# Optimization experiments

Hardware: AMD Instinct MI355X
Metric: run time of the kernel (lower is better)

## Reference

```python
import jax, jax.numpy as jnp
import numpy as np

I_DECAY = 0.95
STAG_THRESH = 0.95
MAX_GATE = 0.6
MIN_I_GATE = 0.25
EPS = 1e-12


def setup_inputs() -> dict:
    key = jax.random.key(0)
    ks = jax.random.split(key, 9)
    B, T, D_IN, D_OUT = 4, 2048, 2048, 2048
    x = jax.random.normal(ks[0], (B, T, D_IN), dtype=jnp.float32)
    s = 1.0 / np.sqrt(D_IN)
    Wp = jax.random.uniform(ks[1], (D_IN, D_OUT), jnp.float32, -s, s)
    Wi = jax.random.uniform(ks[2], (D_IN, D_OUT), jnp.float32, -s, s) * 0.3
    Wd = jax.random.uniform(ks[3], (D_IN, D_OUT), jnp.float32, -s, s) * 0.3
    gate_w = jax.random.uniform(ks[4], (D_IN, 3), jnp.float32, -s, s)
    gate_b = jnp.array([0.5, 0.0, 0.0], dtype=jnp.float32)
    kick_vec = jax.random.normal(ks[5], (D_OUT,), dtype=jnp.float32) * 0.01
    kick_w = jax.random.uniform(ks[6], (D_IN, 1), jnp.float32, -s, s)
    kick_b = jnp.full((1,), -2.0, dtype=jnp.float32)
    bias = jnp.zeros((D_OUT,), dtype=jnp.float32)
    return {"x": x, "Wp": Wp, "Wi": Wi, "Wd": Wd, "gate_w": gate_w,
            "gate_b": gate_b, "kick_vec": kick_vec, "kick_w": kick_w,
            "kick_b": kick_b, "bias": bias}


def _ema_integral(x, decay):
    # x: [B,T,D] -> time-major scan; integral[0] = x[0]
    xt = jnp.swapaxes(x, 0, 1)  # [T,B,D]

    def step(carry, xcur):
        new = decay * carry + (1.0 - decay) * xcur
        return new, new

    init = xt[0]
    _, rest = jax.lax.scan(step, init, xt[1:])
    integral = jnp.concatenate([init[None], rest], axis=0)
    return jnp.swapaxes(integral, 0, 1)  # [B,T,D]


def reference(x, Wp, Wi, Wd, gate_w, gate_b, kick_vec, kick_w, kick_b, bias):
    B, T, D = x.shape
    # --- EMA integral (linear recurrence over T) ---
    integral = _ema_integral(x, I_DECAY)

    # --- stagnation-aware derivative ---
    diff = jnp.concatenate(
        [jnp.zeros_like(x[:, :1]), x[:, 1:] - x[:, :-1]], axis=1)
    x_norm = x / jnp.maximum(
        jnp.linalg.norm(x, axis=-1, keepdims=True), EPS)
    cos_sim = jnp.concatenate(
        [jnp.zeros((B, 1), x.dtype),
         jnp.sum(x_norm[:, 1:] * x_norm[:, :-1], axis=-1)], axis=1)  # [B,T]
    stagnation = (cos_sim > STAG_THRESH).astype(x.dtype)
    kick_strength = jax.nn.sigmoid(
        jnp.einsum('btd,do->bto', x, kick_w) + kick_b)[..., 0]  # [B,T]
    derivative = diff + (stagnation * kick_strength)[..., None] * kick_vec

    # --- gates: softmax -> clamp max -> clamp I min -> renormalize ---
    g = jax.nn.softmax(jnp.einsum('btd,dg->btg', x, gate_w) + gate_b, axis=-1)
    g = jnp.minimum(g, MAX_GATE)
    g = g.at[..., 1].set(jnp.maximum(g[..., 1], MIN_I_GATE))
    g = g / jnp.sum(g, axis=-1, keepdims=True)

    out = (g[..., 0:1] * jnp.einsum('btd,do->bto', x, Wp)
           + g[..., 1:2] * jnp.einsum('btd,do->bto', integral, Wi)
           + g[..., 2:3] * jnp.einsum('btd,do->bto', derivative, Wd))
    return out + bias
```

## Files before the change

### kernel.cpp

```cpp
#include <hip/hip_runtime.h>

#define DH 2048
#define TT 2048
#define BB 4
#define MROWS 8192
#define NZ 6144
#define NCH 128
#define LCH 16
#define LAM 0.44012667f
#define LAM2 1.982646e-06f

typedef __attribute__((ext_vector_type(8))) short bf16x8;
typedef __attribute__((ext_vector_type(4))) float f32x4;

__device__ __forceinline__ unsigned short f2bf(float f) {
  union { float f; unsigned int u; } v; v.f = f;
  unsigned int u = v.u;
  return (unsigned short)((u + 0x7FFFu + ((u >> 16) & 1u)) >> 16);
}
__device__ __forceinline__ float bf2f(unsigned short u) {
  union { unsigned int i; float f; } v; v.i = ((unsigned int)u) << 16;
  return v.f;
}
__device__ __forceinline__ void gld16(const unsigned short* g, unsigned short* l) {
  __builtin_amdgcn_global_load_lds((const __attribute__((address_space(1))) void*)g,
                                   (__attribute__((address_space(3))) void*)l, 16, 0, 0);
}

__global__ __launch_bounds__(256) void prep_w(const float* __restrict__ Wp,
                                              const float* __restrict__ Wi,
                                              const float* __restrict__ Wd,
                                              const float* __restrict__ kick_vec,
                                              unsigned short* __restrict__ Wt,
                                              float* __restrict__ kvWd) {
  __shared__ float tile[64][65];
  int bid = blockIdx.x;
  int mat = bid >> 10;
  int t2 = bid & 1023;
  int dt = (t2 >> 5) * 64;
  int ot = (t2 & 31) * 64;
  const float* W = (mat == 0) ? Wp : ((mat == 1) ? Wi : Wd);
  int nbase = mat * DH;
  int tid = threadIdx.x;
  int r = tid >> 4;
  int c4 = (tid & 15) * 4;
#pragma unroll
  for (int i = 0; i < 4; ++i) {
    int rr = r + i * 16;
    float4 v = *(const float4*)&W[(size_t)(dt + rr) * DH + ot + c4];
    tile[rr][c4 + 0] = v.x; tile[rr][c4 + 1] = v.y;
    tile[rr][c4 + 2] = v.z; tile[rr][c4 + 3] = v.w;
  }
  __syncthreads();
  int o = tid >> 3;
  int d8 = (tid & 7) * 8;
#pragma unroll
  for (int pass = 0; pass < 2; ++pass) {
    int oo = o + pass * 32;
    union { unsigned short u[8]; uint4 v; } pk;
#pragma unroll
    for (int i = 0; i < 8; ++i) pk.u[i] = f2bf(tile[d8 + i][oo]);
    *(uint4*)&Wt[(size_t)(nbase + ot + oo) * DH + dt + d8] = pk.v;
  }
  if (mat == 2 && tid < 64) {
    float s = 0.f;
#pragma unroll 8
    for (int dd = 0; dd < 64; ++dd) s += kick_vec[dt + dd] * tile[dd][tid];
    atomicAdd(&kvWd[ot + tid], s);
  }
}

__global__ __launch_bounds__(256) void conv_x(const float* __restrict__ x,
                                              const float* __restrict__ gate_w,
                                              const float* __restrict__ gate_b,
                                              const float* __restrict__ kick_w,
                                              const float* __restrict__ kick_b,
                                              float* __restrict__ rs,
                                              unsigned short* __restrict__ A) {
  int r = blockIdx.x;
  int t = r & (TT - 1);
  const float* xr = x + (size_t)r * DH;
  const float* xq = xr - DH;
  const bool hp = (t != 0);
  int tid = threadIdx.x;
  float a0 = 0, a1 = 0, a2 = 0, ak = 0, axx = 0, apx = 0, app = 0;
#pragma unroll
  for (int it = 0; it < 2; ++it) {
    int d0 = (tid + it * 256) * 4;
    float4 xv = *(const float4*)(xr + d0);
    float4 pv = hp ? *(const float4*)(xq + d0) : make_float4(0.f, 0.f, 0.f, 0.f);
    float4 q0 = *(const float4*)(gate_w + (size_t)d0 * 3);
    float4 q1 = *(const float4*)(gate_w + (size_t)d0 * 3 + 4);
    float4 q2 = *(const float4*)(gate_w + (size_t)d0 * 3 + 8);
    float4 kw = *(const float4*)(kick_w + d0);
    float xa[4] = {xv.x, xv.y, xv.z, xv.w};
    float pa[4] = {pv.x, pv.y, pv.z, pv.w};
    a0 += xa[0] * q0.x + xa[1] * q0.w + xa[2] * q1.z + xa[3] * q2.y;
    a1 += xa[0] * q0.y + xa[1] * q1.x + xa[2] * q1.w + xa[3] * q2.z;
    a2 += xa[0] * q0.z + xa[1] * q1.y + xa[2] * q2.x + xa[3] * q2.w;
    ak += xa[0] * kw.x + xa[1] * kw.y + xa[2] * kw.z + xa[3] * kw.w;
    union { unsigned short u[4]; uint2 v; } pk;
#pragma unroll
    for (int j = 0; j < 4; ++j) {
      axx += xa[j] * xa[j];
      apx += xa[j] * pa[j];
      app += pa[j] * pa[j];
      pk.u[j] = f2bf(xa[j]);
    }
    *(uint2*)&A[(size_t)r * DH + d0] = pk.v;
  }
#pragma unroll
  for (int off = 32; off > 0; off >>= 1) {
    a0 += __shfl_xor(a0, off); a1 += __shfl_xor(a1, off);
    a2 += __shfl_xor(a2, off); ak += __shfl_xor(ak, off);
    axx += __shfl_xor(axx, off); apx += __shfl_xor(apx, off);
    app += __shfl_xor(app, off);
  }
  __shared__ float red[4][7];
  int wv = tid >> 6;
  if ((tid & 63) == 0) {
    red[wv][0] = a0; red[wv][1] = a1; red[wv][2] = a2; red[wv][3] = ak;
    red[wv][4] = axx; red[wv][5] = apx; red[wv][6] = app;
  }
  __syncthreads();
  if (tid == 0) {
    float v[7];
#pragma unroll
    for (int i = 0; i < 7; ++i) v[i] = red[0][i] + red[1][i] + red[2][i] + red[3][i];
    float l0 = v[0] + gate_b[0], l1 = v[1] + gate_b[1], l2 = v[2] + gate_b[2];
    float mx = fmaxf(l0, fmaxf(l1, l2));
    float e0 = expf(l0 - mx), e1 = expf(l1 - mx), e2 = expf(l2 - mx);
    float inv = 1.f / (e0 + e1 + e2);
    float G0 = fminf(e0 * inv, 0.6f);
    float G1 = fminf(e1 * inv, 0.6f);
    float G2 = fminf(e2 * inv, 0.6f);
    G1 = fmaxf(G1, 0.25f);
    float inv2 = 1.f / (G0 + G1 + G2);
    G0 *= inv2; G1 *= inv2; G2 *= inv2;
    float ks = 1.f / (1.f + expf(-(v[3] + kick_b[0])));
    float nn = fmaxf(sqrtf(v[4]), 1e-12f) * fmaxf(sqrtf(v[6]), 1e-12f);
    float cs = hp ? (v[5] / nn) : 0.f;
    float cc = (cs > 0.95f) ? (G2 * ks) : 0.f;
    *(float4*)(rs + (size_t)r * 4) = make_float4(G0, G1, G2, cc);
  }
}


#define BAR __builtin_amdgcn_s_barrier()
#define VMW6 asm volatile("s_waitcnt vmcnt(6)" ::: "memory")
#define VMW4 asm volatile("s_waitcnt vmcnt(4)" ::: "memory")
#define VMW0 asm volatile("s_waitcnt vmcnt(0)" ::: "memory")
#define LGK8 asm volatile("s_waitcnt lgkmcnt(8)" ::: "memory")
#define LGK0 asm volatile("s_waitcnt lgkmcnt(0)" ::: "memory")

#define ST_A(bf, h, kt) do { \
  gld16(pA + (size_t)((h) * 64) * DH + (kt) * 64,       lA + (bf) * 16384 + (h) * 8192 + ldsW); \
  gld16(pA + (size_t)((h) * 64 + 128) * DH + (kt) * 64, lA + (bf) * 16384 + (h) * 8192 + 4096 + ldsW); \
} while (0)
#define ST_B(bf, g, kt) do { \
  gld16(pB + (size_t)((g) * 32) * DH + (kt) * 64,       lB + (bf) * 16384 + (g) * 8192 + ldsW); \
  gld16(pB + (size_t)((g) * 32 + 128) * DH + (kt) * 64, lB + (bf) * 16384 + (g) * 8192 + 4096 + ldsW); \
} while (0)

#define RD_A(bf, h) do { \
  const unsigned short* p_ = lA + (bf) * 16384 + (h) * 8192 + aRd; \
  _Pragma("unroll") \
  for (int mi_ = 0; mi_ < 4; ++mi_) { \
    av[mi_][0] = *(const bf16x8*)(p_ + mi_ * 1024 + kph0); \
    av[mi_][1] = *(const bf16x8*)(p_ + mi_ * 1024 + kph1); \
  } \
} while (0)
#define RD_B(bf, g) do { \
  const unsigned short* p_ = lB + (bf) * 16384 + (g) * 8192 + bRd; \
  _Pragma("unroll") \
  for (int ni_ = 0; ni_ < 2; ++ni_) { \
    bv[g][ni_][0] = *(const bf16x8*)(p_ + ni_ * 1024 + kph0); \
    bv[g][ni_][1] = *(const bf16x8*)(p_ + ni_ * 1024 + kph1); \
  } \
} while (0)

#define MM(h, g) do { \
  __builtin_amdgcn_s_setprio(1); \
  _Pragma("unroll") \
  for (int mi_ = 0; mi_ < 4; ++mi_) { \
    _Pragma("unroll") \
    for (int ni_ = 0; ni_ < 2; ++ni_) { \
      f32x4 c_ = acc[(h) * 4 + mi_][(g) * 2 + ni_]; \
      c_ = __builtin_amdgcn_mfma_f32_16x16x32_bf16(av[mi_][0], bv[g][ni_][0], c_, 0, 0, 0); \
      c_ = __builtin_amdgcn_mfma_f32_16x16x32_bf16(av[mi_][1], bv[g][ni_][1], c_, 0, 0, 0); \
      acc[(h) * 4 + mi_][(g) * 2 + ni_] = c_; \
    } \
  } \
  __builtin_amdgcn_s_setprio(0); \
} while (0)

__global__ __launch_bounds__(512, 2) void gemm_kernel(const unsigned short* __restrict__ A,
                                                      const unsigned short* __restrict__ Bt,
                                                      unsigned short* __restrict__ Z,
                                                      unsigned short* __restrict__ cpb) {
  __shared__ __align__(16) unsigned short lA[2 * 16384];
  __shared__ __align__(16) unsigned short lB[2 * 16384];
  const int tid = threadIdx.x;
  const int wave = tid >> 6, lane = tid & 63;
  const int bid = blockIdx.x;
  const int xcd = bid & 7;
  const int loc = bid >> 3;
  const int mblk = xcd * 4 + (loc & 3);
  const int nblk = loc >> 2;
  const int m0 = mblk * 256, n0 = nblk * 256;

  const int wm = wave >> 2, wn = wave & 3;
  const int rA = lane & 15, q = lane >> 4, sw = lane & 7;
  const int kph0 = ((0 + q) ^ sw) * 8;
  const int kph1 = ((4 + q) ^ sw) * 8;
  const int aRd = wm * 4096 + rA * 64;
  const int bRd = wn * 2048 + rA * 64;

  const int trow = tid >> 3;
  const int tcol = ((tid & 7) ^ (trow & 7)) * 8;
  const unsigned short* pA = A + (size_t)(m0 + trow) * DH + tcol;
  const unsigned short* pB = Bt + (size_t)(n0 + (trow >> 5) * 64 + (trow & 31)) * DH + tcol;
  const int ldsW = wave * 512;

  bf16x8 av[4][2];
  bf16x8 bv[2][2][2];
  f32x4 acc[8][4] = {};

  ST_A(0, 0, 0); ST_B(0, 0, 0); ST_B(0, 1, 0); ST_A(0, 1, 0);
  ST_A(1, 0, 1); ST_B(1, 0, 1); ST_B(1, 1, 1);
  VMW6; BAR;

#pragma unroll 1
  for (int i = 0; i < 15; ++i) {
    const int t1 = 2 * i + 1, t2 = 2 * i + 2, t3 = 2 * i + 3;
    RD_A(0, 0); RD_B(0, 0); LGK8; BAR; LGK0; MM(0, 0); ST_A(1, 1, t1);
    RD_B(0, 1);                   BAR; LGK0; MM(0, 1); ST_A(0, 0, t2);
    RD_A(0, 1);                   BAR; LGK0; MM(1, 0); ST_B(0, 0, t2);
                            VMW4; BAR;       MM(1, 1); ST_B(0, 1, t2);
    RD_A(1, 0); RD_B(1, 0); LGK8; BAR; LGK0; MM(0, 0); ST_A(0, 1, t2);
    RD_B(1, 1);                   BAR; LGK0; MM(0, 1); ST_A(1, 0, t3);
    RD_A(1, 1);                   BAR; LGK0; MM(1, 0); ST_B(1, 0, t3);
                            VMW4; BAR;       MM(1, 1); ST_B(1, 1, t3);
  }
  RD_A(0, 0); RD_B(0, 0); LGK8; BAR; LGK0; MM(0, 0); ST_A(1, 1, 31);
  RD_B(0, 1);                   BAR; LGK0; MM(0, 1);
  RD_A(0, 1);                   BAR; LGK0; MM(1, 0);
                          VMW0; BAR;       MM(1, 1);
  RD_A(1, 0); RD_B(1, 0); LGK8; BAR; LGK0; MM(0, 0);
  RD_B(1, 1);                   BAR; LGK0; MM(0, 1);
  RD_A(1, 1);                   BAR; LGK0; MM(1, 0);
                                           MM(1, 1);

  const int mbase = m0 + wm * 128;
  const int nbase = n0 + wn * 64;

  if (nblk >= 8 && nblk < 16) {
    float w12 = (q == 3) ? 1.0f : (q == 2) ? 0.81450625f
              : (q == 1) ? 0.66342043f : 0.54036009f;
    w12 *= 0.05f;
#pragma unroll
    for (int mi = 0; mi < 8; ++mi) {
      const int mrow = mbase + mi * 16;
      const int bb = mrow >> 11;
      const int chh = (mrow >> 4) & (NCH - 1);
      const bool first = (chh == 0);
#pragma unroll
      for (int ni = 0; ni < 4; ++ni) {
        float v0 = acc[mi][ni][0];
        float s = ((v0 * 0.95f + acc[mi][ni][1]) * 0.95f + acc[mi][ni][2]) * 0.95f
                  + acc[mi][ni][3];
        if (first && q == 0) s += 19.0f * 0.857375f * v0;
        s *= w12;
        s += __shfl_xor(s, 16);
        s += __shfl_xor(s, 32);
        if (q == 0) {
          int nloc = nbase + ni * 16 + rA - 2048;
          cpb[((size_t)bb * NCH + chh) * DH + nloc] = f2bf(s);
        }
      }
    }
  }

#pragma unroll
  for (int mi = 0; mi < 8; ++mi) {
#pragma unroll
    for (int rg = 0; rg < 4; ++rg) {
      const int m = mbase + mi * 16 + q * 4 + rg;
#pragma unroll
      for (int ni = 0; ni < 4; ++ni) {
        const int n = nbase + ni * 16 + rA;
        Z[(size_t)m * NZ + n] = f2bf(acc[mi][ni][rg]);
      }
    }
  }
}

#undef BAR
#undef VMW6
#undef VMW4
#undef VMW0
#undef LGK8
#undef LGK0
#undef ST_A
#undef ST_B
#undef RD_A
#undef RD_B
#undef MM

__global__ __launch_bounds__(256) void zi_p1(unsigned short* __restrict__ cpb,
                                             float* __restrict__ gc) {
  int gid = blockIdx.x * 256 + threadIdx.x;
  int n = gid & (DH - 1);
  int g = (gid >> 11) & 7;
  int b = gid >> 14;
  float run = 0.f;
#pragma unroll
  for (int j = 0; j < 16; ++j) {
    size_t idx = ((size_t)b * NCH + g * 16 + j) * DH + n;
    float c = bf2f(cpb[idx]);
    cpb[idx] = f2bf(run);
    run = c + LAM * run;
  }
  gc[((size_t)b * 8 + g) * DH + n] = run;
}

__global__ __launch_bounds__(256) void zi_p2(float* __restrict__ gc) {
  int gid = blockIdx.x * 256 + threadIdx.x;
  int n = gid & (DH - 1);
  int b = gid >> 11;
  float run = 0.f;
#pragma unroll
  for (int g = 0; g < 8; ++g) {
    size_t idx = ((size_t)b * 8 + g) * DH + n;
    float old = gc[idx];
    gc[idx] = run;
    run = old + LAM2 * run;
  }
}

__global__ __launch_bounds__(256) void final_combine(const unsigned short* __restrict__ Z,
                                                     const float* __restrict__ rs,
                                                     const unsigned short* __restrict__ cpb,
                                                     const float* __restrict__ gc,
                                                     const float* __restrict__ kvWd,
                                                     const float* __restrict__ bias,
                                                     float* __restrict__ out) {
  int tid = threadIdx.x;
  int n = blockIdx.y * 1024 + tid * 4;
  int ch = blockIdx.x & (NCH - 1);
  int b = blockIdx.x >> 7;
  int r0 = b * TT + ch * LCH;
  const unsigned short* zb = Z + (size_t)r0 * NZ + n;
  const bool first_chunk = (ch == 0);

  int g = ch >> 4, j = ch & 15;
  float pw = 1.f;
  for (int i = 0; i < j; ++i) pw *= LAM;
  float Pv[4];
  {
    union { unsigned short u[4]; uint2 v; } c;
    c.v = *(const uint2*)&cpb[((size_t)b * NCH + ch) * DH + n];
    float4 gp = *(const float4*)&gc[((size_t)b * 8 + g) * DH + n];
    float gpa[4] = {gp.x, gp.y, gp.z, gp.w};
#pragma unroll
    for (int i = 0; i < 4; ++i) Pv[i] = bf2f(c.u[i]) + pw * gpa[i];
  }
  float kv[4], bz[4];
  {
    float4 k0 = *(const float4*)&kvWd[n];
    float4 b0 = *(const float4*)&bias[n];
    kv[0]=k0.x; kv[1]=k0.y; kv[2]=k0.z; kv[3]=k0.w;
    bz[0]=b0.x; bz[1]=b0.y; bz[2]=b0.z; bz[3]=b0.w;
  }
  float zdp[4];
  if (!first_chunk) {
    union { unsigned short u[4]; uint2 v; } c;
    c.v = *(const uint2*)(zb - NZ + 2 * DH);
#pragma unroll
    for (int i = 0; i < 4; ++i) zdp[i] = bf2f(c.u[i]);
  } else {
#pragma unroll
    for (int i = 0; i < 4; ++i) zdp[i] = 0.f;
  }
  float J[4];
#pragma unroll
  for (int i = 0; i < 4; ++i) J[i] = 0.f;
  float f = 1.f;
  uint2 cp = *(const uint2*)(zb);
  uint2 ci = *(const uint2*)(zb + DH);
  uint2 cd = *(const uint2*)(zb + 2 * DH);
#pragma unroll
  for (int tau = 0; tau < LCH; ++tau) {
    uint2 np, ni, nd;
    if (tau < LCH - 1) {
      const unsigned short* zn = zb + (size_t)(tau + 1) * NZ;
      np = *(const uint2*)(zn);
      ni = *(const uint2*)(zn + DH);
      nd = *(const uint2*)(zn + 2 * DH);
    }
    float4 gg = *(const float4*)&rs[(size_t)(r0 + tau) * 4];
    union { unsigned short u[4]; uint2 v; } up, ui, ud;
    up.v = cp; ui.v = ci; ud.v = cd;
    const bool vfirst = first_chunk && (tau == 0);
    f *= 0.95f;
    float o[4];
#pragma unroll
    for (int i = 0; i < 4; ++i) {
      float xp = bf2f(up.u[i]), xi = bf2f(ui.u[i]), xd = bf2f(ud.u[i]);
      if (vfirst) J[i] = xi;
      else J[i] = 0.95f * J[i] + 0.05f * xi;
      float I = J[i] + f * Pv[i];
      float diff = vfirst ? 0.f : (xd - zdp[i]);
      o[i] = gg.x * xp + gg.y * I + gg.z * diff + gg.w * kv[i] + bz[i];
      zdp[i] = xd;
    }
    *(float4*)(out + (size_t)(r0 + tau) * DH + n) = make_float4(o[0], o[1], o[2], o[3]);
    cp = np; ci = ni; cd = nd;
  }
}

extern "C" void kernel_launch(void* const* d_in, const int* in_sizes, int n_in,
                              void* d_out, int out_size, void* d_ws, size_t ws_size,
                              hipStream_t stream) {
  const float* x        = (const float*)d_in[0];
  const float* Wp       = (const float*)d_in[1];
  const float* Wi       = (const float*)d_in[2];
  const float* Wd       = (const float*)d_in[3];
  const float* gate_w   = (const float*)d_in[4];
  const float* gate_b   = (const float*)d_in[5];
  const float* kick_vec = (const float*)d_in[6];
  const float* kick_w   = (const float*)d_in[7];
  const float* kick_b   = (const float*)d_in[8];
  const float* bias     = (const float*)d_in[9];
  float* out = (float*)d_out;

  char* ws = (char*)d_ws;
  unsigned short* Wt  = (unsigned short*)(ws + 0);
  unsigned short* Z   = (unsigned short*)(ws + 25165824);
  float* rs   = (float*)(ws + 125829120);
  float* kvWd = (float*)(ws + 125960192);
  unsigned short* cpb = (unsigned short*)(ws + 125968384);
  float* gc   = (float*)(ws + 128065536);
  unsigned short* A = (unsigned short*)d_out;
  (void)ws_size; (void)in_sizes; (void)n_in; (void)out_size;

  hipMemsetAsync(kvWd, 0, DH * sizeof(float), stream);
  prep_w<<<dim3(3072), dim3(256), 0, stream>>>(Wp, Wi, Wd, kick_vec, Wt, kvWd);
  conv_x<<<dim3(8192), dim3(256), 0, stream>>>(x, gate_w, gate_b, kick_w, kick_b, rs, A);
  gemm_kernel<<<dim3(768), dim3(512), 0, stream>>>(A, Wt, Z, cpb);
  zi_p1<<<dim3(256), dim3(256), 0, stream>>>(cpb, gc);
  zi_p2<<<dim3(32), dim3(256), 0, stream>>>(gc);
  final_combine<<<dim3(512, 2), dim3(256), 0, stream>>>(Z, rs, cpb, gc, kvWd, bias, out);
}
```

Baseline: 373.3 us.

## Merge prep kernels, drop zi_p2 pass, reorder GEMM LDS stores before waits

Merges the weight-transpose and x-conversion kernels into one launch with a block-index split, which removes one kernel launch and lets the two independent prep jobs overlap. It drops the second-level carry scan kernel and computes the group carry inline in final_combine from the two previous group carries. Because LAM2 is about 2e-6, terms beyond two groups back are treated as negligible, so this is an approximation of the full scan. It also reorders the GEMM main loop so the next global-to-LDS stores are issued right after the barrier and before the LDS wait and MFMA, and removes the partial lgkmcnt(8) wait.

```diff
diff --git a/kernel.cpp b/kernel.cpp
--- a/kernel.cpp
+++ b/kernel.cpp
@@ -27,62 +27,63 @@
                                    (__attribute__((address_space(3))) void*)l, 16, 0, 0);
 }
 
-__global__ __launch_bounds__(256) void prep_w(const float* __restrict__ Wp,
-                                              const float* __restrict__ Wi,
-                                              const float* __restrict__ Wd,
-                                              const float* __restrict__ kick_vec,
-                                              unsigned short* __restrict__ Wt,
-                                              float* __restrict__ kvWd) {
+__global__ __launch_bounds__(256) void prep_conv(const float* __restrict__ Wp,
+                                                 const float* __restrict__ Wi,
+                                                 const float* __restrict__ Wd,
+                                                 const float* __restrict__ kick_vec,
+                                                 unsigned short* __restrict__ Wt,
+                                                 float* __restrict__ kvWd,
+                                                 const float* __restrict__ x,
+                                                 const float* __restrict__ gate_w,
+                                                 const float* __restrict__ gate_b,
+                                                 const float* __restrict__ kick_w,
+                                                 const float* __restrict__ kick_b,
+                                                 float* __restrict__ rs,
+                                                 unsigned short* __restrict__ A) {
   __shared__ float tile[64][65];
+  __shared__ float red[4][7];
   int bid = blockIdx.x;
-  int mat = bid >> 10;
-  int t2 = bid & 1023;
-  int dt = (t2 >> 5) * 64;
-  int ot = (t2 & 31) * 64;
-  const float* W = (mat == 0) ? Wp : ((mat == 1) ? Wi : Wd);
-  int nbase = mat * DH;
   int tid = threadIdx.x;
-  int r = tid >> 4;
-  int c4 = (tid & 15) * 4;
-#pragma unroll
-  for (int i = 0; i < 4; ++i) {
-    int rr = r + i * 16;
-    float4 v = *(const float4*)&W[(size_t)(dt + rr) * DH + ot + c4];
-    tile[rr][c4 + 0] = v.x; tile[rr][c4 + 1] = v.y;
-    tile[rr][c4 + 2] = v.z; tile[rr][c4 + 3] = v.w;
-  }
-  __syncthreads();
-  int o = tid >> 3;
-  int d8 = (tid & 7) * 8;
-#pragma unroll
-  for (int pass = 0; pass < 2; ++pass) {
-    int oo = o + pass * 32;
-    union { unsigned short u[8]; uint4 v; } pk;
-#pragma unroll
-    for (int i = 0; i < 8; ++i) pk.u[i] = f2bf(tile[d8 + i][oo]);
-    *(uint4*)&Wt[(size_t)(nbase + ot + oo) * DH + dt + d8] = pk.v;
-  }
-  if (mat == 2 && tid < 64) {
-    float s = 0.f;
+  if (bid < 3072) {
+    int mat = bid >> 10;
+    int t2 = bid & 1023;
+    int dt = (t2 >> 5) * 64;
+    int ot = (t2 & 31) * 64;
+    const float* W = (mat == 0) ? Wp : ((mat == 1) ? Wi : Wd);
+    int nbase = mat * DH;
+    int r = tid >> 4;
+    int c4 = (tid & 15) * 4;
+#pragma unroll
+    for (int i = 0; i < 4; ++i) {
+      int rr = r + i * 16;
+      float4 v = *(const float4*)&W[(size_t)(dt + rr) * DH + ot + c4];
+      tile[rr][c4 + 0] = v.x; tile[rr][c4 + 1] = v.y;
+      tile[rr][c4 + 2] = v.z; tile[rr][c4 + 3] = v.w;
+    }
+    __syncthreads();
+    int o = tid >> 3;
+    int d8 = (tid & 7) * 8;
+#pragma unroll
+    for (int pass = 0; pass < 2; ++pass) {
+      int oo = o + pass * 32;
+      union { unsigned short u[8]; uint4 v; } pk;
+#pragma unroll
+      for (int i = 0; i < 8; ++i) pk.u[i] = f2bf(tile[d8 + i][oo]);
+      *(uint4*)&Wt[(size_t)(nbase + ot + oo) * DH + dt + d8] = pk.v;
+    }
+    if (mat == 2 && tid < 64) {
+      float s = 0.f;
 #pragma unroll 8
-    for (int dd = 0; dd < 64; ++dd) s += kick_vec[dt + dd] * tile[dd][tid];
-    atomicAdd(&kvWd[ot + tid], s);
-  }
-}
-
-__global__ __launch_bounds__(256) void conv_x(const float* __restrict__ x,
-                                              const float* __restrict__ gate_w,
-                                              const float* __restrict__ gate_b,
-                                              const float* __restrict__ kick_w,
-                                              const float* __restrict__ kick_b,
-                                              float* __restrict__ rs,
-                                              unsigned short* __restrict__ A) {
-  int r = blockIdx.x;
+      for (int dd = 0; dd < 64; ++dd) s += kick_vec[dt + dd] * tile[dd][tid];
+      atomicAdd(&kvWd[ot + tid], s);
+    }
+    return;
+  }
+  int r = bid - 3072;
   int t = r & (TT - 1);
   const float* xr = x + (size_t)r * DH;
   const float* xq = xr - DH;
   const bool hp = (t != 0);
-  int tid = threadIdx.x;
   float a0 = 0, a1 = 0, a2 = 0, ak = 0, axx = 0, apx = 0, app = 0;
 #pragma unroll
   for (int it = 0; it < 2; ++it) {
@@ -116,7 +117,6 @@
     axx += __shfl_xor(axx, off); apx += __shfl_xor(apx, off);
     app += __shfl_xor(app, off);
   }
-  __shared__ float red[4][7];
   int wv = tid >> 6;
   if ((tid & 63) == 0) {
     red[wv][0] = a0; red[wv][1] = a1; red[wv][2] = a2; red[wv][3] = ak;
@@ -150,7 +150,6 @@
 #define VMW6 asm volatile("s_waitcnt vmcnt(6)" ::: "memory")
 #define VMW4 asm volatile("s_waitcnt vmcnt(4)" ::: "memory")
 #define VMW0 asm volatile("s_waitcnt vmcnt(0)" ::: "memory")
-#define LGK8 asm volatile("s_waitcnt lgkmcnt(8)" ::: "memory")
 #define LGK0 asm volatile("s_waitcnt lgkmcnt(0)" ::: "memory")
 
 #define ST_A(bf, h, kt) do { \
@@ -233,23 +232,23 @@
 #pragma unroll 1
   for (int i = 0; i < 15; ++i) {
     const int t1 = 2 * i + 1, t2 = 2 * i + 2, t3 = 2 * i + 3;
-    RD_A(0, 0); RD_B(0, 0); LGK8; BAR; LGK0; MM(0, 0); ST_A(1, 1, t1);
-    RD_B(0, 1);                   BAR; LGK0; MM(0, 1); ST_A(0, 0, t2);
-    RD_A(0, 1);                   BAR; LGK0; MM(1, 0); ST_B(0, 0, t2);
-                            VMW4; BAR;       MM(1, 1); ST_B(0, 1, t2);
-    RD_A(1, 0); RD_B(1, 0); LGK8; BAR; LGK0; MM(0, 0); ST_A(0, 1, t2);
-    RD_B(1, 1);                   BAR; LGK0; MM(0, 1); ST_A(1, 0, t3);
-    RD_A(1, 1);                   BAR; LGK0; MM(1, 0); ST_B(1, 0, t3);
-                            VMW4; BAR;       MM(1, 1); ST_B(1, 1, t3);
-  }
-  RD_A(0, 0); RD_B(0, 0); LGK8; BAR; LGK0; MM(0, 0); ST_A(1, 1, 31);
-  RD_B(0, 1);                   BAR; LGK0; MM(0, 1);
-  RD_A(0, 1);                   BAR; LGK0; MM(1, 0);
-                          VMW0; BAR;       MM(1, 1);
-  RD_A(1, 0); RD_B(1, 0); LGK8; BAR; LGK0; MM(0, 0);
-  RD_B(1, 1);                   BAR; LGK0; MM(0, 1);
-  RD_A(1, 1);                   BAR; LGK0; MM(1, 0);
-                                           MM(1, 1);
+    RD_A(0, 0); RD_B(0, 0); BAR; ST_A(1, 1, t1); LGK0; MM(0, 0);
+    RD_B(0, 1);             BAR; ST_A(0, 0, t2); LGK0; MM(0, 1);
+    RD_A(0, 1);             BAR; ST_B(0, 0, t2); LGK0; MM(1, 0);
+                      VMW4; BAR; ST_B(0, 1, t2);       MM(1, 1);
+    RD_A(1, 0); RD_B(1, 0); BAR; ST_A(0, 1, t2); LGK0; MM(0, 0);
+    RD_B(1, 1);             BAR; ST_A(1, 0, t3); LGK0; MM(0, 1);
+    RD_A(1, 1);             BAR; ST_B(1, 0, t3); LGK0; MM(1, 0);
+                      VMW4; BAR; ST_B(1, 1, t3);       MM(1, 1);
+  }
+  RD_A(0, 0); RD_B(0, 0); BAR; ST_A(1, 1, 31); LGK0; MM(0, 0);
+  RD_B(0, 1);             BAR;                 LGK0; MM(0, 1);
+  RD_A(0, 1);             BAR;                 LGK0; MM(1, 0);
+                    VMW0; BAR;                       MM(1, 1);
+  RD_A(1, 0); RD_B(1, 0); BAR;                 LGK0; MM(0, 0);
+  RD_B(1, 1);             BAR;                 LGK0; MM(0, 1);
+  RD_A(1, 1);             BAR;                 LGK0; MM(1, 0);
+                                                     MM(1, 1);
 
   const int mbase = m0 + wm * 128;
   const int nbase = n0 + wn * 64;
@@ -299,7 +298,6 @@
 #undef VMW6
 #undef VMW4
 #undef VMW0
-#undef LGK8
 #undef LGK0
 #undef ST_A
 #undef ST_B
@@ -322,20 +320,6 @@
     run = c + LAM * run;
   }
   gc[((size_t)b * 8 + g) * DH + n] = run;
-}
-
-__global__ __launch_bounds__(256) void zi_p2(float* __restrict__ gc) {
-  int gid = blockIdx.x * 256 + threadIdx.x;
-  int n = gid & (DH - 1);
-  int b = gid >> 11;
-  float run = 0.f;
-#pragma unroll
-  for (int g = 0; g < 8; ++g) {
-    size_t idx = ((size_t)b * 8 + g) * DH + n;
-    float old = gc[idx];
-    gc[idx] = run;
-    run = old + LAM2 * run;
-  }
 }
 
 __global__ __launch_bounds__(256) void final_combine(const unsigned short* __restrict__ Z,
@@ -360,8 +344,16 @@
   {
     union { unsigned short u[4]; uint2 v; } c;
     c.v = *(const uint2*)&cpb[((size_t)b * NCH + ch) * DH + n];
-    float4 gp = *(const float4*)&gc[((size_t)b * 8 + g) * DH + n];
-    float gpa[4] = {gp.x, gp.y, gp.z, gp.w};
+    float gpa[4] = {0.f, 0.f, 0.f, 0.f};
+    if (g >= 1) {
+      float4 g1 = *(const float4*)&gc[((size_t)b * 8 + g - 1) * DH + n];
+      gpa[0] = g1.x; gpa[1] = g1.y; gpa[2] = g1.z; gpa[3] = g1.w;
+    }
+    if (g >= 2) {
+      float4 g2 = *(const float4*)&gc[((size_t)b * 8 + g - 2) * DH + n];
+      gpa[0] += LAM2 * g2.x; gpa[1] += LAM2 * g2.y;
+      gpa[2] += LAM2 * g2.z; gpa[3] += LAM2 * g2.w;
+    }
 #pragma unroll
     for (int i = 0; i < 4; ++i) Pv[i] = bf2f(c.u[i]) + pw * gpa[i];
   }
@@ -445,10 +437,9 @@
   (void)ws_size; (void)in_sizes; (void)n_in; (void)out_size;
 
   hipMemsetAsync(kvWd, 0, DH * sizeof(float), stream);
-  prep_w<<<dim3(3072), dim3(256), 0, stream>>>(Wp, Wi, Wd, kick_vec, Wt, kvWd);
-  conv_x<<<dim3(8192), dim3(256), 0, stream>>>(x, gate_w, gate_b, kick_w, kick_b, rs, A);
+  prep_conv<<<dim3(11264), dim3(256), 0, stream>>>(Wp, Wi, Wd, kick_vec, Wt, kvWd,
+                                                   x, gate_w, gate_b, kick_w, kick_b, rs, A);
   gemm_kernel<<<dim3(768), dim3(512), 0, stream>>>(A, Wt, Z, cpb);
   zi_p1<<<dim3(256), dim3(256), 0, stream>>>(cpb, gc);
-  zi_p2<<<dim3(32), dim3(256), 0, stream>>>(gc);
   final_combine<<<dim3(512, 2), dim3(256), 0, stream>>>(Z, rs, cpb, gc, kvWd, bias, out);
 }
```

New measurement: 369.3 us. No clear change (-1.1%).
